# Optimization experiments

Measured on AMD Instinct MI355X. Metric: run time of the kernel, lower is better.

Reference implementation:

```python
import jax, jax.numpy as jnp
import numpy as np

T = 5       # fixed temporal factor in the original forward
HEADS = 8
DIM = 512
DIM_HEAD = 64
INNER = HEADS * DIM_HEAD  # 512 (must equal DIM for the masked scatter)


def setup_inputs() -> dict:
    key = jax.random.key(0)
    ks = jax.random.split(key, 8)
    bt, n = 40, 3137  # b=8, t=5; n-1 = 56*56 visual tokens
    x = jax.random.normal(ks[0], (bt, n, DIM), dtype=jnp.float32)
    mask = jax.random.randint(ks[1], (bt, 56, 56), 0, 2).astype(jnp.float32)
    s = 1.0 / np.sqrt(DIM)
    w_vq = jax.random.normal(ks[2], (DIM, INNER), dtype=jnp.float32) * s
    w_vkv = jax.random.normal(ks[3], (DIM, 2 * INNER), dtype=jnp.float32) * s
    w_aqkv = jax.random.normal(ks[4], (DIM, 3 * INNER), dtype=jnp.float32) * s
    w_out = jax.random.normal(ks[5], (INNER, DIM), dtype=jnp.float32) * s
    b_out = jnp.zeros((DIM,), dtype=jnp.float32)
    return {"x": x, "mask": mask, "w_vq": w_vq, "w_vkv": w_vkv,
            "w_aqkv": w_aqkv, "w_out": w_out, "b_out": b_out}


def reference(x, mask, w_vq, w_vkv, w_aqkv, w_out, b_out):
    bt, n, dim = x.shape
    b = bt // T
    nv = n - 1
    dh = DIM_HEAD
    scale = dh ** -0.5

    A = x[:, 0]        # (bt, dim) -- single 'action' token per frame
    V = x[:, 1:]       # (bt, nv, dim)
    m = mask.reshape(bt, nv, 1)

    aq, ak, av = jnp.split(A @ w_aqkv, 3, axis=-1)      # each (bt, INNER)
    vk, vv = jnp.split(V @ w_vkv, 2, axis=-1)           # each (bt, nv, INNER)
    vq = V @ w_vq                                        # (bt, nv, INNER)

    # --- A -> V cross attention: per batch, T A-queries over T*nv V keys ---
    qa = aq.reshape(b, T, HEADS, dh)
    Kv = vk.reshape(b, T * nv, HEADS, dh)
    Vv = vv.reshape(b, T * nv, HEADS, dh)
    av_dots = jnp.einsum('bqhd,bkhd->bhqk', qa, Kv) * scale
    av_attn = jax.nn.softmax(av_dots, axis=-1)
    av_o = jnp.einsum('bhqk,bkhd->bqhd', av_attn, Vv)   # (b, T, H, dh)
    a_out = av_o.reshape(bt, 1, INNER)

    # --- V -> A cross attention with block mask: every V token attends only
    # to its own batch's T A-tokens (the -inf block fill in the original) ---
    Qv = vq.reshape(b, T, nv, HEADS, dh)
    Ka = ak.reshape(b, T, HEADS, dh)
    Va = av.reshape(b, T, HEADS, dh)
    va_dots = jnp.einsum('bfnhd,bkhd->bhfnk', Qv, Ka) * scale
    va_attn = jax.nn.softmax(va_dots, axis=-1)          # softmax over T keys
    va_o = jnp.einsum('bhfnk,bkhd->bfnhd', va_attn, Va)
    v_full = va_o.reshape(bt, nv, INNER)

    # original: scatter attn out into V.clone() then * mask, under no_grad()
    # => masked positions get attention output, others V*0 = 0; detached.
    v_out = jax.lax.stop_gradient(v_full * m)

    out = jnp.concatenate([a_out, v_out], axis=1)       # (bt, n, INNER)
    return out @ w_out + b_out
```

## Files before the change

kernel.cpp:

```cpp
#include <hip/hip_runtime.h>

typedef unsigned short u16;
typedef unsigned int u32;
typedef __attribute__((ext_vector_type(8))) u16 u16x8;
typedef __attribute__((ext_vector_type(8))) __bf16 bf16x8;
typedef __attribute__((ext_vector_type(4))) float f32x4;

__device__ __forceinline__ float b2f(u16 u){ return __uint_as_float(((u32)u)<<16); }
__device__ __forceinline__ u16 f2b(float f){
  u32 b = __float_as_uint(f);
  return (u16)((b + 0x7fffu + ((b>>16)&1u))>>16);
}
__device__ __forceinline__ void gload16(const void* g, void* l){
  __builtin_amdgcn_global_load_lds((__attribute__((address_space(1))) void*)g,
                                   (__attribute__((address_space(3))) void*)l, 16, 0, 0);
}
__device__ __forceinline__ float wred_max(float v){
#pragma unroll
  for (int o=32;o>0;o>>=1) v = fmaxf(v, __shfl_xor(v,o));
  return v;
}
__device__ __forceinline__ float wred_sum(float v){
#pragma unroll
  for (int o=32;o>0;o>>=1) v += __shfl_xor(v,o);
  return v;
}



__global__ void k_pre(const float* __restrict__ x, const float* __restrict__ wvq,
                      const float* __restrict__ wvkv, const float* __restrict__ wout,
                      const float* __restrict__ waqkv,
                      u16* __restrict__ xb, u16* __restrict__ W1T,
                      u16* __restrict__ WoutT, float* __restrict__ aqkv){
  const int bid = blockIdx.x, tid = threadIdx.x;
  if (bid < 2048){
    const int stride = 2048*256;
    for (int i = bid*256 + tid; i < 8030720; i += stride){
      const float4* p = (const float4*)(x + (size_t)i*8);
      float4 a = p[0], b = p[1];
      u16x8 o;
      o[0]=f2b(a.x); o[1]=f2b(a.y); o[2]=f2b(a.z); o[3]=f2b(a.w);
      o[4]=f2b(b.x); o[5]=f2b(b.y); o[6]=f2b(b.z); o[7]=f2b(b.w);
      *(u16x8*)(xb + (size_t)i*8) = o;
    }
  } else if (bid < 6144){
    int id = (bid-2048)*256 + tid;
    if (id < 786432){
      int n = id >> 9, k = id & 511;
      float v;
      if (n < 512){
        v = wvq[k*512 + n];
      } else {
        int j = n - 512, h = j >> 7, r = j & 127;
        int c2 = (r < 64) ? (h*64 + r) : (512 + h*64 + (r - 64));
        v = wvkv[k*1024 + c2];
      }
      W1T[id] = f2b(v);
    } else {
      int j = id - 786432;
      int n = j >> 9, k = j & 511;
      WoutT[j] = f2b(wout[k*512 + n]);
    }
  } else {
    int id = (bid-6144)*256 + tid;
    int bt = id / 1536, c = id % 1536;
    const float* xr = x + (size_t)bt*3137*512;
    float s = 0.f;
    for (int k=0;k<512;k++) s += xr[k]*waqkv[k*1536+c];
    aqkv[id] = s;
  }
}

template<int FOUT>
__global__ __launch_bounds__(512, 2) void k_gemm256(
    const u16* __restrict__ A, const u16* __restrict__ BT,
    int M, int N, int K, int NX,
    u16* __restrict__ Cb, float* __restrict__ Cf, const float* __restrict__ bias)
{
  __shared__ __align__(16) char Ls[4][32768];
  const int tid = threadIdx.x;
  const int wid = tid >> 6, lane = tid & 63;
  const int nwg = gridDim.x, orig = blockIdx.x;
  const int q8 = nwg >> 3, r8 = nwg & 7;
  const int xc = orig & 7, sl = orig >> 3;
  const int work = (xc < r8 ? xc*(q8+1) : r8*(q8+1) + (xc-r8)*q8) + sl;
  const int m0 = (work / NX) * 256, n0 = (work % NX) * 256;
  const size_t K2 = (size_t)K * 2;
  const char* Ab = (const char*)A;
  const char* Bb = (const char*)BT;
  size_t asrc[2], bsrc[2];
  const int ad0 = wid*1024, ad1 = 8192 + wid*1024;
#pragma unroll
  for (int i=0;i<2;i++){
    int row = (i*8 + wid)*16 + (lane & 15);
    int koff = (lane >> 4) << 4;
    int ra = m0 + row; if (ra >= M) ra = M - 1;
    asrc[i] = (size_t)ra * K2 + koff;
    bsrc[i] = (size_t)(n0 + row) * K2 + koff;
  }
#define STAGE(s4, ks) { \
    size_t ko = (size_t)(ks) * 64; \
    gload16(Ab + asrc[0] + ko, Ls[s4] + ad0); \
    gload16(Ab + asrc[1] + ko, Ls[s4] + ad1); \
    gload16(Bb + bsrc[0] + ko, Ls[s4] + 16384 + ad0); \
    gload16(Bb + bsrc[1] + ko, Ls[s4] + 16384 + ad1); }

  f32x4 acc[8][4] = {};
  const int awb = (wid >> 2) * 8192;
  const int bwb = 16384 + (wid & 3) * 4096;
  const int NS = K >> 5;
  STAGE(0,0) STAGE(1,1) STAGE(2,2)
  for (int s = 0; s < NS; ++s){
    if (s + 2 < NS)      { asm volatile("s_waitcnt vmcnt(8)" ::: "memory"); }
    else if (s + 1 < NS) { asm volatile("s_waitcnt vmcnt(4)" ::: "memory"); }
    else                 { asm volatile("s_waitcnt vmcnt(0)" ::: "memory"); }
    __builtin_amdgcn_s_barrier();
    __builtin_amdgcn_sched_barrier(0);
    if (s + 3 < NS) STAGE((s+3)&3, s+3)
    const char* base = Ls[s & 3];
    bf16x8 af[8], bfr[4];
#pragma unroll
    for (int i=0;i<4;i++) af[i]  = *(const bf16x8*)(base + awb + i*1024 + lane*16);
#pragma unroll
    for (int i=0;i<4;i++) bfr[i] = *(const bf16x8*)(base + bwb + i*1024 + lane*16);
    asm volatile("s_waitcnt lgkmcnt(0)" ::: "memory");
    __builtin_amdgcn_sched_barrier(0);
    __builtin_amdgcn_s_setprio(1);
#pragma unroll
    for (int mr=0;mr<4;mr++)
#pragma unroll
      for (int nc=0;nc<4;nc++)
        acc[mr][nc] = __builtin_amdgcn_mfma_f32_16x16x32_bf16(af[mr], bfr[nc], acc[mr][nc], 0,0,0);
    __builtin_amdgcn_s_setprio(0);
#pragma unroll
    for (int i=4;i<8;i++) af[i] = *(const bf16x8*)(base + awb + i*1024 + lane*16);
    asm volatile("s_waitcnt lgkmcnt(0)" ::: "memory");
    __builtin_amdgcn_sched_barrier(0);
    __builtin_amdgcn_s_setprio(1);
#pragma unroll
    for (int mr=4;mr<8;mr++)
#pragma unroll
      for (int nc=0;nc<4;nc++)
        acc[mr][nc] = __builtin_amdgcn_mfma_f32_16x16x32_bf16(af[mr], bfr[nc], acc[mr][nc], 0,0,0);
    __builtin_amdgcn_s_setprio(0);
  }
#undef STAGE
  const int wm = (wid >> 2) * 128, wn = (wid & 3) * 64;
  if (m0 + 256 <= M){
#pragma unroll
    for (int mr=0;mr<8;mr++){
#pragma unroll
      for (int nc=0;nc<4;nc++){
#pragma unroll
        for (int rg=0;rg<4;rg++){
          int row = m0 + wm + mr*16 + ((lane>>4)<<2) + rg;
          int col = n0 + wn + nc*16 + (lane&15);
          float v = acc[mr][nc][rg];
          if (FOUT) Cf[(size_t)row*N + col] = v + bias[col];
          else      Cb[(size_t)row*N + col] = f2b(v);
        }
      }
    }
  } else {
#pragma unroll
    for (int mr=0;mr<8;mr++){
#pragma unroll
      for (int nc=0;nc<4;nc++){
#pragma unroll
        for (int rg=0;rg<4;rg++){
          int row = m0 + wm + mr*16 + ((lane>>4)<<2) + rg;
          int col = n0 + wn + nc*16 + (lane&15);
          if (row < M){
            float v = acc[mr][nc][rg];
            if (FOUT) Cf[(size_t)row*N + col] = v + bias[col];
            else      Cb[(size_t)row*N + col] = f2b(v);
          }
        }
      }
    }
  }
}

__global__ __launch_bounds__(320) void k_attn_agent(
    const u16* __restrict__ out1, const float* __restrict__ aqkv,
    float* __restrict__ pm, float* __restrict__ pl, float* __restrict__ pacc)
{
  __shared__ __align__(16) char Ksm[16384];
  __shared__ __align__(16) char Vsm[16384];
  const int bid = blockIdx.x;
  const int sp = bid & 15, bh = bid >> 4, b = bh >> 3, h = bh & 7;
  const int tid = threadIdx.x, wid = tid >> 6, lane = tid & 63;
  const int q = wid;
  float qreg[64];
  {
    const float* ap = aqkv + ((size_t)(b*5+q)*1536 + h*64);
#pragma unroll
    for (int d=0; d<64; d++) qreg[d] = ap[d];
  }
  float m = -1e30f, l = 0.f;
  float acc[8] = {0,0,0,0,0,0,0,0};
  const int g0 = sp * 980;
  for (int c = 0; c < 8; c++){
    for (int idx = tid; idx < 2048; idx += 320){
      int r = idx >> 4, g = idx & 15;
      int loc = c*128 + r; if (loc > 979) loc = 979;
      int gk = g0 + loc;
      int tk = gk / 3136, nv = gk - tk*3136;
      size_t grow = (size_t)((b*5+tk)*3137 + 1 + nv)*1536 + 512 + h*128 + g*8;
      u16x8 v = *(const u16x8*)(out1 + grow);
      char* dst = (g < 8) ? Ksm : Vsm;
      int seg = g & 7;
      *(u16x8*)(dst + r*128 + ((seg*16) ^ ((r&7)<<4))) = v;
    }
    __syncthreads();
    float s0 = 0.f, s1 = 0.f;
#pragma unroll
    for (int seg=0; seg<8; seg++){
      const int r0 = lane, r1 = 64 + lane;
      u16x8 k0 = *(const u16x8*)(Ksm + r0*128 + ((seg*16) ^ ((r0&7)<<4)));
      u16x8 k1 = *(const u16x8*)(Ksm + r1*128 + ((seg*16) ^ ((r1&7)<<4)));
#pragma unroll
      for (int j=0;j<8;j++){
        s0 += qreg[seg*8+j]*b2f(k0[j]);
        s1 += qreg[seg*8+j]*b2f(k1[j]);
      }
    }
    s0 *= 0.125f; s1 *= 0.125f;
    const int locbase = c*128;
    if (locbase + lane >= 980)      s0 = -1e30f;
    if (locbase + 64 + lane >= 980) s1 = -1e30f;
    float cmax = wred_max(fmaxf(s0, s1));
    float mn = fmaxf(m, cmax);
    float resc = __expf(m - mn);
    float p0 = (s0 > -1e29f) ? __expf(s0 - mn) : 0.f;
    float p1 = (s1 > -1e29f) ? __expf(s1 - mn) : 0.f;
    l = l*resc + wred_sum(p0 + p1);
#pragma unroll
    for (int j=0;j<8;j++) acc[j] *= resc;
    const int g = lane >> 3, cc = lane & 7;
#pragma unroll
    for (int i=0;i<16;i++){
      int k = i*8 + g;
      u16x8 vv = *(const u16x8*)(Vsm + k*128 + ((cc*16) ^ ((k&7)<<4)));
      float p = (i < 8) ? __shfl(p0, k) : __shfl(p1, k-64);
#pragma unroll
      for (int j=0;j<8;j++) acc[j] += p*b2f(vv[j]);
    }
    m = mn;
    __syncthreads();
  }
#pragma unroll
  for (int j=0;j<8;j++){
    float v = acc[j];
    v += __shfl_xor(v, 8); v += __shfl_xor(v, 16); v += __shfl_xor(v, 32);
    acc[j] = v;
  }
  const int base = (bh*16 + sp)*5 + q;
  if (lane == 0){ pm[base] = m; pl[base] = l; }
  if (lane < 8){
    float* pa = pacc + (size_t)base*64 + lane*8;
#pragma unroll
    for (int j=0;j<8;j++) pa[j] = acc[j];
  }
}

__global__ __launch_bounds__(256) void k_attn_frame(
    const u16* __restrict__ out1, const float* __restrict__ aqkv,
    const float* __restrict__ mask, const float* __restrict__ pm,
    const float* __restrict__ pl, const float* __restrict__ pacc,
    u16* __restrict__ IN)
{
  const int bid = blockIdx.x, tid = threadIdx.x;
  if (bid < 3920){
    __shared__ float Ka[5][8][68];
    __shared__ float Va[5][8][68];
    const int b = bid / 490, bx = bid % 490;
    for (int i = tid; i < 2560; i += 256){
      int t = i >> 9, rem = i & 511, hh = rem >> 6, d = rem & 63;
      const float* src = aqkv + (size_t)(b*5+t)*1536;
      Ka[t][hh][d] = src[512 + hh*64 + d];
      Va[t][hh][d] = src[1024 + hh*64 + d];
    }
    __syncthreads();
    const int task = bx*256 + tid;
    const int h = task & 7, rl = task >> 3;
    const int f = rl / 3136, nv = rl - f*3136;
    const int bt = b*5 + f;
    const size_t r1 = (size_t)bt*3137 + 1 + nv;
    const u16* qp = out1 + r1*1536 + h*64;
    float qf[64];
#pragma unroll
    for (int sg=0; sg<8; sg++){
      u16x8 v = *(const u16x8*)(qp + sg*8);
#pragma unroll
      for (int j=0;j<8;j++) qf[sg*8+j] = b2f(v[j]);
    }
    float sd[5];
#pragma unroll
    for (int t=0;t<5;t++){
      float s = 0.f;
#pragma unroll
      for (int d=0;d<64;d++) s += qf[d]*Ka[t][h][d];
      sd[t] = s*0.125f;
    }
    float mx = sd[0];
#pragma unroll
    for (int t=1;t<5;t++) mx = fmaxf(mx, sd[t]);
    float p[5], ps = 0.f;
#pragma unroll
    for (int t=0;t<5;t++){ p[t] = __expf(sd[t]-mx); ps += p[t]; }
    const float mv = mask[(size_t)bt*3136 + nv] / ps;
    u16* op = IN + r1*512 + h*64;
#pragma unroll
    for (int sg=0; sg<8; sg++){
      u16x8 o;
#pragma unroll
      for (int j=0;j<8;j++){
        const int d = sg*8+j;
        float v = 0.f;
#pragma unroll
        for (int t=0;t<5;t++) v += p[t]*Va[t][h][d];
        o[j] = f2b(v*mv);
      }
      *(u16x8*)(op + sg*8) = o;
    }
  } else {
    const int id = (bid - 3920)*4 + (tid >> 6);
    const int d = tid & 63;
    const int q = id % 5, t2 = id / 5;
    const int h = t2 & 7, b = t2 >> 3;
    const int bh = b*8 + h;
    float ms = -1e30f;
#pragma unroll
    for (int s2=0;s2<16;s2++) ms = fmaxf(ms, pm[(bh*16+s2)*5+q]);
    float L = 0.f, o = 0.f;
#pragma unroll
    for (int s2=0;s2<16;s2++){
      int base = (bh*16+s2)*5+q;
      float w = __expf(pm[base]-ms);
      L += w*pl[base];
      o += w*pacc[(size_t)base*64 + d];
    }
    IN[(size_t)(b*5+q)*3137*512 + h*64 + d] = f2b(o / L);
  }
}

extern "C" void kernel_launch(void* const* d_in, const int* in_sizes, int n_in,
                              void* d_out, int out_size, void* d_ws, size_t ws_size,
                              hipStream_t stream)
{
  const float* x      = (const float*)d_in[0];
  const float* mask   = (const float*)d_in[1];
  const float* w_vq   = (const float*)d_in[2];
  const float* w_vkv  = (const float*)d_in[3];
  const float* w_aqkv = (const float*)d_in[4];
  const float* w_out  = (const float*)d_in[5];
  const float* b_out  = (const float*)d_in[6];
  float* out = (float*)d_out;
  char* ws = (char*)d_ws;

  constexpr size_t MR = 125480;
  constexpr size_t OFF_XB   = 0;
  constexpr size_t OFF_OUT1 = OFF_XB + MR*512*2;
  constexpr size_t OFF_W1T  = OFF_OUT1 + MR*1536*2;
  constexpr size_t OFF_WOT  = OFF_W1T + 1536*512*2;
  constexpr size_t OFF_AQKV = OFF_WOT + 512*512*2;
  constexpr size_t OFF_PM   = OFF_AQKV + 40*1536*4;
  constexpr size_t OFF_PL   = OFF_PM + 5120*4;
  constexpr size_t OFF_PACC = OFF_PL + 5120*4;

  u16* Xb     = (u16*)(ws + OFF_XB);
  u16* out1   = (u16*)(ws + OFF_OUT1);
  u16* W1T    = (u16*)(ws + OFF_W1T);
  u16* WoutT  = (u16*)(ws + OFF_WOT);
  float* aqkv = (float*)(ws + OFF_AQKV);
  float* pm   = (float*)(ws + OFF_PM);
  float* pl   = (float*)(ws + OFF_PL);
  float* pacc = (float*)(ws + OFF_PACC);

  k_pre<<<6384, 256, 0, stream>>>(x, w_vq, w_vkv, w_out, w_aqkv, Xb, W1T, WoutT, aqkv);
  k_gemm256<0><<<2946, 512, 0, stream>>>(Xb, W1T, (int)MR, 1536, 512, 6,
                                         out1, nullptr, nullptr);
  k_attn_agent<<<1024, 320, 0, stream>>>(out1, aqkv, pm, pl, pacc);
  k_attn_frame<<<4000, 256, 0, stream>>>(out1, aqkv, mask, pm, pl, pacc, Xb);
  k_gemm256<1><<<982, 512, 0, stream>>>(Xb, WoutT, (int)MR, 512, 512, 2,
                                        nullptr, out, b_out);
}
```

Before: 783.4 us.

## Restructure bf16 GEMM into 8-phase quadrant-pipelined schedule with K=64 tiles

Replaces the 4-stage K=32 ring-buffer GEMM main loop with an 8-phase schedule. Each 128-row or 128-col half-tile of A and B is staged separately into a double buffer of K=64 tiles. Global-to-LDS loads for the next tiles are issued between per-quadrant MFMA phases, each phase separated by barriers, so memory traffic overlaps compute at a finer grain. Warp-to-output mapping changes to 2x4 quadrant subtiles, and the store indexing is updated to match. It adds more barriers per K step and uses 128KB of LDS per block, which may limit occupancy to one block per CU.

```diff
diff --git a/kernel.cpp b/kernel.cpp
--- a/kernel.cpp
+++ b/kernel.cpp
@@ -25,7 +25,6 @@
   for (int o=32;o>0;o>>=1) v += __shfl_xor(v,o);
   return v;
 }
-
 
 
 __global__ void k_pre(const float* __restrict__ x, const float* __restrict__ wvq,
@@ -73,14 +72,17 @@
 }
 
 template<int FOUT>
-__global__ __launch_bounds__(512, 2) void k_gemm256(
+__global__ __launch_bounds__(512, 2) void k_gemm8p(
     const u16* __restrict__ A, const u16* __restrict__ BT,
     int M, int N, int K, int NX,
     u16* __restrict__ Cb, float* __restrict__ Cf, const float* __restrict__ bias)
 {
-  __shared__ __align__(16) char Ls[4][32768];
+  __shared__ __align__(16) char Ls[131072];
+  char* LA = Ls;
+  char* LB = Ls + 65536;
   const int tid = threadIdx.x;
   const int wid = tid >> 6, lane = tid & 63;
+  const int wm = wid >> 2, wn = wid & 3;
   const int nwg = gridDim.x, orig = blockIdx.x;
   const int q8 = nwg >> 3, r8 = nwg & 7;
   const int xc = orig & 7, sl = orig >> 3;
@@ -89,92 +91,118 @@
   const size_t K2 = (size_t)K * 2;
   const char* Ab = (const char*)A;
   const char* Bb = (const char*)BT;
-  size_t asrc[2], bsrc[2];
-  const int ad0 = wid*1024, ad1 = 8192 + wid*1024;
-#pragma unroll
-  for (int i=0;i<2;i++){
-    int row = (i*8 + wid)*16 + (lane & 15);
-    int koff = (lane >> 4) << 4;
-    int ra = m0 + row; if (ra >= M) ra = M - 1;
-    asrc[i] = (size_t)ra * K2 + koff;
-    bsrc[i] = (size_t)(n0 + row) * K2 + koff;
-  }
-#define STAGE(s4, ks) { \
-    size_t ko = (size_t)(ks) * 64; \
-    gload16(Ab + asrc[0] + ko, Ls[s4] + ad0); \
-    gload16(Ab + asrc[1] + ko, Ls[s4] + ad1); \
-    gload16(Bb + bsrc[0] + ko, Ls[s4] + 16384 + ad0); \
-    gload16(Bb + bsrc[1] + ko, Ls[s4] + 16384 + ad1); }
+  size_t asrch[2], bsrch[2];
+#pragma unroll
+  for (int h=0; h<2; h++){
+    int ra = m0 + h*128 + wid*16 + (lane & 15);
+    if (ra >= M) ra = M - 1;
+    asrch[h] = (size_t)ra * K2 + ((lane >> 4) << 4);
+    bsrch[h] = (size_t)(n0 + h*128 + wid*16 + (lane & 15)) * K2 + ((lane >> 4) << 4);
+  }
+  const int sd0 = wid*2048;
+
+#define STG_A(d,h,kt) { size_t ko = (size_t)(kt)*128; \
+    gload16(Ab + asrch[h] + ko,      LA + (d)*32768 + (h)*16384 + sd0); \
+    gload16(Ab + asrch[h] + ko + 64, LA + (d)*32768 + (h)*16384 + sd0 + 1024); }
+#define STG_B(d,h,kt) { size_t ko = (size_t)(kt)*128; \
+    gload16(Bb + bsrch[h] + ko,      LB + (d)*32768 + (h)*16384 + sd0); \
+    gload16(Bb + bsrch[h] + ko + 64, LB + (d)*32768 + (h)*16384 + sd0 + 1024); }
+
+  bf16x8 afr[4][2], bfr[2][2];
+#define RD_A(d,QM) { const char* ab_ = LA + (d)*32768 + (QM)*16384 + wm*8192 + lane*16; \
+    _Pragma("unroll") for (int fm=0; fm<4; fm++){ \
+      afr[fm][0] = *(const bf16x8*)(ab_ + fm*2048); \
+      afr[fm][1] = *(const bf16x8*)(ab_ + fm*2048 + 1024); } }
+#define RD_B(d,QN) { const char* bb_ = LB + (d)*32768 + (QN)*16384 + wn*4096 + lane*16; \
+    _Pragma("unroll") for (int fn=0; fn<2; fn++){ \
+      bfr[fn][0] = *(const bf16x8*)(bb_ + fn*2048); \
+      bfr[fn][1] = *(const bf16x8*)(bb_ + fn*2048 + 1024); } }
 
   f32x4 acc[8][4] = {};
-  const int awb = (wid >> 2) * 8192;
-  const int bwb = 16384 + (wid & 3) * 4096;
-  const int NS = K >> 5;
-  STAGE(0,0) STAGE(1,1) STAGE(2,2)
-  for (int s = 0; s < NS; ++s){
-    if (s + 2 < NS)      { asm volatile("s_waitcnt vmcnt(8)" ::: "memory"); }
-    else if (s + 1 < NS) { asm volatile("s_waitcnt vmcnt(4)" ::: "memory"); }
-    else                 { asm volatile("s_waitcnt vmcnt(0)" ::: "memory"); }
-    __builtin_amdgcn_s_barrier();
+#define MFMA16(QM,QN) { \
+    _Pragma("unroll") for (int fm=0; fm<4; fm++){ \
+      _Pragma("unroll") for (int fn=0; fn<2; fn++){ \
+        acc[(QM)*4+fm][(QN)*2+fn] = __builtin_amdgcn_mfma_f32_16x16x32_bf16( \
+            afr[fm][0], bfr[fn][0], acc[(QM)*4+fm][(QN)*2+fn], 0,0,0); \
+        acc[(QM)*4+fm][(QN)*2+fn] = __builtin_amdgcn_mfma_f32_16x16x32_bf16( \
+            afr[fm][1], bfr[fn][1], acc[(QM)*4+fm][(QN)*2+fn], 0,0,0); } } }
+
+#define PH_MID(QM,QN) \
+    __builtin_amdgcn_sched_barrier(0); \
+    __builtin_amdgcn_s_barrier(); \
+    asm volatile("s_waitcnt lgkmcnt(0)" ::: "memory"); \
+    __builtin_amdgcn_sched_barrier(0); \
+    __builtin_amdgcn_s_setprio(1); \
+    MFMA16(QM,QN) \
+    __builtin_amdgcn_s_setprio(0); \
     __builtin_amdgcn_sched_barrier(0);
-    if (s + 3 < NS) STAGE((s+3)&3, s+3)
-    const char* base = Ls[s & 3];
-    bf16x8 af[8], bfr[4];
-#pragma unroll
-    for (int i=0;i<4;i++) af[i]  = *(const bf16x8*)(base + awb + i*1024 + lane*16);
-#pragma unroll
-    for (int i=0;i<4;i++) bfr[i] = *(const bf16x8*)(base + bwb + i*1024 + lane*16);
-    asm volatile("s_waitcnt lgkmcnt(0)" ::: "memory");
-    __builtin_amdgcn_sched_barrier(0);
-    __builtin_amdgcn_s_setprio(1);
-#pragma unroll
-    for (int mr=0;mr<4;mr++)
-#pragma unroll
-      for (int nc=0;nc<4;nc++)
-        acc[mr][nc] = __builtin_amdgcn_mfma_f32_16x16x32_bf16(af[mr], bfr[nc], acc[mr][nc], 0,0,0);
-    __builtin_amdgcn_s_setprio(0);
-#pragma unroll
-    for (int i=4;i<8;i++) af[i] = *(const bf16x8*)(base + awb + i*1024 + lane*16);
-    asm volatile("s_waitcnt lgkmcnt(0)" ::: "memory");
-    __builtin_amdgcn_sched_barrier(0);
-    __builtin_amdgcn_s_setprio(1);
-#pragma unroll
-    for (int mr=4;mr<8;mr++)
-#pragma unroll
-      for (int nc=0;nc<4;nc++)
-        acc[mr][nc] = __builtin_amdgcn_mfma_f32_16x16x32_bf16(af[mr], bfr[nc], acc[mr][nc], 0,0,0);
-    __builtin_amdgcn_s_setprio(0);
-  }
-#undef STAGE
-  const int wm = (wid >> 2) * 128, wn = (wid & 3) * 64;
+#define BAR __builtin_amdgcn_s_barrier()
+
+  const int NI = K >> 7;
+  STG_A(0,0,0) STG_B(0,1,0) STG_A(0,1,0) STG_B(0,0,0) STG_A(1,0,1) STG_B(1,1,1)
+  asm volatile("s_waitcnt vmcnt(4)" ::: "memory");
+  BAR;
+
+  for (int it = 0; it < NI; ++it){
+    const int t1 = 2*it + 1, t2 = 2*it + 2, t3 = 2*it + 3;
+    const bool more = (it + 1 < NI);
+    RD_A(0,0) RD_B(0,0) STG_A(1,1,t1)
+    PH_MID(0,0) BAR;
+    RD_B(0,1) STG_B(1,0,t1)
+    PH_MID(0,1) BAR;
+    RD_A(0,1) if (more){ STG_A(0,0,t2) }
+    PH_MID(1,1) BAR;
+    RD_B(0,0) if (more){ STG_B(0,1,t2) }
+    PH_MID(1,0)
+    if (more) { asm volatile("s_waitcnt vmcnt(4)" ::: "memory"); }
+    else      { asm volatile("s_waitcnt vmcnt(0)" ::: "memory"); }
+    BAR;
+    RD_A(1,0) RD_B(1,0) if (more){ STG_A(0,1,t2) }
+    PH_MID(0,0) BAR;
+    RD_B(1,1) if (more){ STG_B(0,0,t2) }
+    PH_MID(0,1) BAR;
+    RD_A(1,1) if (more){ STG_A(1,0,t3) }
+    PH_MID(1,1) BAR;
+    RD_B(1,0) if (more){ STG_B(1,1,t3) }
+    PH_MID(1,0)
+    if (more) { asm volatile("s_waitcnt vmcnt(4)" ::: "memory"); }
+    BAR;
+  }
+#undef STG_A
+#undef STG_B
+#undef RD_A
+#undef RD_B
+#undef MFMA16
+#undef PH_MID
+#undef BAR
   if (m0 + 256 <= M){
 #pragma unroll
-    for (int mr=0;mr<8;mr++){
-#pragma unroll
-      for (int nc=0;nc<4;nc++){
-#pragma unroll
-        for (int rg=0;rg<4;rg++){
-          int row = m0 + wm + mr*16 + ((lane>>4)<<2) + rg;
-          int col = n0 + wn + nc*16 + (lane&15);
-          float v = acc[mr][nc][rg];
-          if (FOUT) Cf[(size_t)row*N + col] = v + bias[col];
-          else      Cb[(size_t)row*N + col] = f2b(v);
+    for (int mi=0; mi<8; mi++){
+      const int rb = m0 + (mi>>2)*128 + wm*64 + (mi&3)*16 + ((lane>>4)<<2);
+#pragma unroll
+      for (int ni=0; ni<4; ni++){
+        const int col = n0 + (ni>>1)*128 + wn*32 + (ni&1)*16 + (lane&15);
+#pragma unroll
+        for (int rg=0; rg<4; rg++){
+          float v = acc[mi][ni][rg];
+          if (FOUT) Cf[(size_t)(rb+rg)*N + col] = v + bias[col];
+          else      Cb[(size_t)(rb+rg)*N + col] = f2b(v);
         }
       }
     }
   } else {
 #pragma unroll
-    for (int mr=0;mr<8;mr++){
-#pragma unroll
-      for (int nc=0;nc<4;nc++){
-#pragma unroll
-        for (int rg=0;rg<4;rg++){
-          int row = m0 + wm + mr*16 + ((lane>>4)<<2) + rg;
-          int col = n0 + wn + nc*16 + (lane&15);
-          if (row < M){
-            float v = acc[mr][nc][rg];
-            if (FOUT) Cf[(size_t)row*N + col] = v + bias[col];
-            else      Cb[(size_t)row*N + col] = f2b(v);
+    for (int mi=0; mi<8; mi++){
+      const int rb = m0 + (mi>>2)*128 + wm*64 + (mi&3)*16 + ((lane>>4)<<2);
+#pragma unroll
+      for (int ni=0; ni<4; ni++){
+        const int col = n0 + (ni>>1)*128 + wn*32 + (ni&1)*16 + (lane&15);
+#pragma unroll
+        for (int rg=0; rg<4; rg++){
+          if (rb + rg < M){
+            float v = acc[mi][ni][rg];
+            if (FOUT) Cf[(size_t)(rb+rg)*N + col] = v + bias[col];
+            else      Cb[(size_t)(rb+rg)*N + col] = f2b(v);
           }
         }
       }
@@ -380,10 +408,10 @@
   float* pacc = (float*)(ws + OFF_PACC);
 
   k_pre<<<6384, 256, 0, stream>>>(x, w_vq, w_vkv, w_out, w_aqkv, Xb, W1T, WoutT, aqkv);
-  k_gemm256<0><<<2946, 512, 0, stream>>>(Xb, W1T, (int)MR, 1536, 512, 6,
-                                         out1, nullptr, nullptr);
+  k_gemm8p<0><<<2946, 512, 0, stream>>>(Xb, W1T, (int)MR, 1536, 512, 6,
+                                        out1, nullptr, nullptr);
   k_attn_agent<<<1024, 320, 0, stream>>>(out1, aqkv, pm, pl, pacc);
   k_attn_frame<<<4000, 256, 0, stream>>>(out1, aqkv, mask, pm, pl, pacc, Xb);
-  k_gemm256<1><<<982, 512, 0, stream>>>(Xb, WoutT, (int)MR, 512, 512, 2,
-                                        nullptr, out, b_out);
-}
+  k_gemm8p<1><<<982, 512, 0, stream>>>(Xb, WoutT, (int)MR, 512, 512, 2,
+                                       nullptr, out, b_out);
+}
```

After: 774.6 us. About the same (-1.1%).
